# Optimization experiments

Measured on AMD Instinct MI355X. Metric: run time of the kernel, lower is better.

The kernel has to match this reference:

```python
import jax, jax.numpy as jnp
import numpy as np

B, K, V_DIM, EMBED, HID, NTOKEN, MAX_LEN = 128, 36, 2048, 1024, 1024, 10000, 20


def _u(key, shape, scale=0.05):
    return jax.random.uniform(key, shape, jnp.float32, -scale, scale)


def setup_inputs() -> dict:
    key = jax.random.key(0)
    ks = jax.random.split(key, 12)
    d1 = HID + V_DIM + EMBED  # word_rnn input size
    d2 = V_DIM + HID          # language_rnn input size
    return dict(
        v=jax.random.normal(ks[0], (B, K, V_DIM), jnp.float32),
        caption=jax.random.normal(ks[1], (B, MAX_LEN, EMBED), jnp.float32),
        cap_len=jnp.sort(jax.random.randint(ks[2], (B,), 2, MAX_LEN + 1))[::-1].astype(jnp.int32),
        Wih1=_u(ks[3], (3 * HID, d1)), Whh1=_u(ks[4], (3 * HID, HID)),
        bih1=jnp.zeros((3 * HID,), jnp.float32), bhh1=jnp.zeros((3 * HID,), jnp.float32),
        Wih2=_u(ks[5], (3 * HID, d2)), Whh2=_u(ks[6], (3 * HID, HID)),
        bih2=jnp.zeros((3 * HID,), jnp.float32), bhh2=jnp.zeros((3 * HID,), jnp.float32),
        Wv=_u(ks[7], (HID, V_DIM)), bv=jnp.zeros((HID,), jnp.float32),
        Wq=_u(ks[8], (HID, HID)), bq=jnp.zeros((HID,), jnp.float32),
        wa=_u(ks[9], (HID,)), ba=jnp.zeros((), jnp.float32),
        W1=_u(ks[10], (HID, HID)), b1=jnp.zeros((HID,), jnp.float32),
        W2=_u(ks[11], (NTOKEN, HID)), b2=jnp.zeros((NTOKEN,), jnp.float32),
    )


def _gru(x, h, Wih, Whh, bih, bhh):
    # PyTorch GRUCell math, gate order (r, z, n)
    gi = x @ Wih.T + bih
    gh = h @ Whh.T + bhh
    ir, iz, inn = jnp.split(gi, 3, axis=-1)
    hr, hz, hn = jnp.split(gh, 3, axis=-1)
    r = jax.nn.sigmoid(ir + hr)
    z = jax.nn.sigmoid(iz + hz)
    n = jnp.tanh(inn + r * hn)
    return (1.0 - z) * n + z * h


def reference(v, caption, cap_len, Wih1, Whh1, bih1, bhh1, Wih2, Whh2, bih2, bhh2,
              Wv, bv, Wq, bq, wa, ba, W1, b1, W2, b2):
    # sort by caption length, descending (as torch forward does)
    order = jnp.argsort(-cap_len)
    v = v[order]
    caption = caption[order]
    cap_len = cap_len[order]
    v_mean = v.mean(1)                                  # [B, V_DIM]
    vproj = jax.nn.relu(v @ Wv.T + bv)                  # [B, K, HID], hoisted out of time loop

    T = MAX_LEN - 1
    dl = cap_len - 1                                    # decode lengths
    mask = (jnp.arange(T)[:, None] < dl[None, :]).astype(v.dtype)   # [T, B]
    prevs = jnp.swapaxes(caption[:, :T, :], 0, 1)       # [T, B, EMBED]

    def step(carry, xs):
        h1, h2 = carry
        prev, m = xs
        h1n = _gru(jnp.concatenate([h2, v_mean, prev], axis=1), h1, Wih1, Whh1, bih1, bhh1)
        hq = h1n @ W1.T + b1                            # h1_fcnet (dropout = identity in eval)
        # 'base' attention: softmax over objects of w^T(relu(Wv v) * relu(Wq q))
        logits = (vproj * jax.nn.relu(hq @ Wq.T + bq)[:, None, :]) @ wa + ba   # [B, K]
        att = jax.nn.softmax(logits, axis=1)
        att_v = jnp.einsum('bk,bkd->bd', att, v)        # attended image feature
        h2n = _gru(jnp.concatenate([att_v, hq], axis=1), h2, Wih2, Whh2, bih2, bhh2)
        word = h2n @ W2.T + b2                          # [B, NTOKEN]
        return (h1n, h2n), (word * m[:, None], att * m[:, None])

    init = (jnp.zeros((B, HID), v.dtype), jnp.zeros((B, HID), v.dtype))
    _, (words, atts) = jax.lax.scan(step, init, (prevs, mask))
    # pad back to max_len timesteps as the torch output buffer does
    predict = jnp.pad(jnp.swapaxes(words, 0, 1), ((0, 0), (0, 1), (0, 0)))   # [B, MAX_LEN, NTOKEN]
    alphas = jnp.pad(jnp.swapaxes(atts, 0, 1), ((0, 0), (0, 1), (0, 0)))     # [B, MAX_LEN, K]
    return predict, alphas
```

## Files before the change

kernel.cpp:

```cpp
#include <hip/hip_runtime.h>
#include <hip/hip_cooperative_groups.h>

namespace cg = cooperative_groups;

typedef unsigned short u16;
typedef __attribute__((ext_vector_type(8))) short bf16x8;
typedef __attribute__((ext_vector_type(4))) float f32x4;

#define NB 128
#define NOBJ 36
#define VDIM 2048
#define EMB 1024
#define HID 1024
#define NTOK 10000
#define MAXLEN 20
#define T_STEPS 19
#define PRED_STRIDE (MAXLEN * NTOK)
#define ALPHA_OFF ((long)NB * MAXLEN * NTOK)
#define HSZ (NB * HID)

struct Args {
  const float *v, *caption;
  const int *cap_len;
  const float *Wih1, *Whh1, *bih1, *bhh1, *Wih2, *Whh2, *bih2, *bhh2;
  const float *Wv, *bv, *Wq, *bq, *wa, *ba, *W1, *b1, *W2, *b2;
  float *out;
  int *order, *dl;
  u16 *Wih1h, *Whh1h, *Wih2h, *Whh2h, *Wvh, *W2h, *vh, *caph, *capl;
  u16 *Wqh, *Wql, *W1T, *Wih2hql, *Wq1u, *Wih2qu;
  u16 *vproj16;
  float *gv1, *gh2s, *h1f, *h2f, *qf, *gcap, *g1a, *g1c, *g2a, *g2b, *gi2h1;
  float *bq1f, *bf2f;
  u16 *h1hi, *h1lo, *h2hi, *h2lo, *avhi, *avlo, *vmhi, *vmlo;
};

__device__ inline float b2f(u16 h) {
  unsigned u = ((unsigned)h) << 16;
  float f;
  __builtin_memcpy(&f, &u, 4);
  return f;
}
__device__ inline u16 f2b_trunc(float x) {
  unsigned u;
  __builtin_memcpy(&u, &x, 4);
  return (u16)(u >> 16);
}
__device__ inline u16 f2b_rne(float x) {
  unsigned u;
// ... 22 lines not shown
__device__ inline float tanhf_(float x) {
  float e = __expf(-2.f * fabsf(x));
  float t = (1.f - e) / (1.f + e);
  return x >= 0.f ? t : -t;
}
__device__ inline float wred_sum(float x) {
#pragma unroll
  for (int off = 32; off > 0; off >>= 1) x += __shfl_xor(x, off, 64);
  return x;
}
__device__ inline float wred_max(float x) {
#pragma unroll
  for (int off = 32; off > 0; off >>= 1) x = fmaxf(x, __shfl_xor(x, off, 64));
  return x;
}

__device__ inline void cvt_hi(const float *src, u16 *dst, long n, long g0,
                              long gs) {
  for (long i = g0 * 4; i < n; i += gs * 4) {
    float4 f = *(const float4 *)(src + i);
    ushort4 o;
    o.x = f2b_rne(f.x);
    o.y = f2b_rne(f.y);
    o.z = f2b_rne(f.z);
    o.w = f2b_rne(f.w);
    *(ushort4 *)(dst + i) = o;
  }
}
__device__ inline void cvt_split(const float *src, u16 *dhi, u16 *dlo, long n,
                                 long g0, long gs) {
  for (long i = g0 * 4; i < n; i += gs * 4) {
    float4 f = *(const float4 *)(src + i);
    ushort4 h, l;
    split_bf16(f.x, h.x, l.x);
    split_bf16(f.y, h.y, l.y);
    split_bf16(f.z, h.z, l.z);
    split_bf16(f.w, h.w, l.w);
    *(ushort4 *)(dhi + i) = h;
    *(ushort4 *)(dlo + i) = l;
  }
}

#define MMK_BODY                                                               \
  {                                                                            \
    const int ko = ks * 32;                                                    \
    bf16x8 va = ldb8(ah + ko);                                                 \
    bf16x8 vl;                                                                 \
    if constexpr (SPLIT) vl = ldb8(al + ko);                                   \
    _Pragma("unroll") for (int i = 0; i < NT; ++i) {                           \
      bf16x8 vb = ldb8(wr + (long)i * wstride + ko);                           \
      acc[i] = mfma16(va, vb, acc[i]);                                         \
      if constexpr (SPLIT) acc[i] = mfma16(vl, vb, acc[i]);                    \
    }                                                                          \
  }

template <int NT, bool SPLIT>
__device__ inline void mmk(f32x4 *acc, const u16 *ah, const u16 *al,
                           const u16 *wr, long wstride, int ksteps) {
  if constexpr (NT == 1) {
#pragma unroll 4
    for (int ks = 0; ks < ksteps; ++ks) MMK_BODY
  } else {
#pragma unroll 2
    for (int ks = 0; ks < ksteps; ++ks) MMK_BODY
  }
}

template <bool SPLIT>
__device__ inline f32x4 tile16(const u16 *ah, const u16 *al, const u16 *wr,
                               int K) {
  f32x4 acc = {0.f, 0.f, 0.f, 0.f};
  mmk<1, SPLIT>(&acc, ah, al, wr, 0, K >> 5);
  return acc;
}

__global__ void __launch_bounds__(512, 4) butd(Args a) {
  cg::grid_group grid = cg::this_grid();
  const int tid = threadIdx.x;
  const int blk = blockIdx.x;
  const int gx = gridDim.x;
  const int lane = tid & 63;
  const int wv = tid >> 6;
  const int m = lane & 15;
  const int quad = lane >> 4;
  __shared__ float sl[64];

  const long gs = (long)gx * 512;
  const long g0 = (long)blk * 512 + tid;

  cvt_hi(a.Wih1, a.Wih1h, 3072L * 4096, g0, gs);
  cvt_hi(a.Whh1, a.Whh1h, 3072L * 1024, g0, gs);
  cvt_hi(a.Wih2, a.Wih2h, 3072L * 3072, g0, gs);
  cvt_hi(a.Whh2, a.Whh2h, 3072L * 1024, g0, gs);
  cvt_hi(a.Wv, a.Wvh, 1024L * 2048, g0, gs);
  cvt_hi(a.W2, a.W2h, (long)NTOK * 1024, g0, gs);
  cvt_hi(a.v, a.vh, (long)NB * NOBJ * VDIM, g0, gs);
  cvt_split(a.caption, a.caph, a.capl, (long)NB * MAXLEN * EMB, g0, gs);
  cvt_split(a.Wq, a.Wqh, a.Wql, 1024L * 1024, g0, gs);
  for (long i = g0; i < 1024L * 1024; i += gs) {
    const int ii = (int)(i >> 10), mm2 = (int)(i & 1023);
    a.W1T[i] = f2b_rne(a.W1[(long)mm2 * 1024 + ii]);
  }
  for (long i = g0 * 4; i < 3072L * 1024; i += gs * 4) {
    const int row = (int)(i >> 10), c = (int)(i & 1023);
    float4 f = *(const float4 *)(a.Wih2 + (long)row * 3072 + 2048 + c);
    ushort4 l;
    l.x = f2b_trunc(f.x - b2f(f2b_rne(f.x)));
    l.y = f2b_trunc(f.y - b2f(f2b_rne(f.y)));
    l.z = f2b_trunc(f.z - b2f(f2b_rne(f.z)));
    l.w = f2b_trunc(f.w - b2f(f2b_rne(f.w)));
    *(ushort4 *)(a.Wih2hql + i) = l;
  }

  if (blk == 0 && tid < NB) {
    int ki = a.cap_len[tid];
    int rank = 0;
    for (int j = 0; j < NB; ++j) {
      int kj = a.cap_len[j];
      rank += (kj > ki) || (kj == ki && j < tid);
    }
    a.order[rank] = tid;
    a.dl[rank] = ki - 1;
  }
  for (long i = g0; i < (long)NB * NTOK; i += gs) {
    long b = i / NTOK, n = i - b * NTOK;
    a.out[b * PRED_STRIDE + (long)(MAXLEN - 1) * NTOK + n] = 0.f;
  }
  for (long i = g0; i < (long)NB * NOBJ; i += gs) {
    long b = i / NOBJ, n = i - b * NOBJ;
    a.out[ALPHA_OFF + b * (MAXLEN * NOBJ) + (MAXLEN - 1) * NOBJ + n] = 0.f;
  }
  for (long i = g0; i < HSZ; i += gs) {
    a.h1f[i] = 0.f;
    a.h2f[i] = 0.f;
    a.h1hi[i] = 0;
    a.h1lo[i] = 0;
    a.h2hi[i] = 0;
    a.h2lo[i] = 0;
  }
  for (long i = g0; i < 128L * 3072; i += gs) a.g1c[i] = 0.f;
  grid.sync();

  for (int b = blk; b < NB; b += gx) {
    const int ob = a.order[b];
    const float *vb = a.v + (long)ob * NOBJ * VDIM;
    for (int d = tid; d < VDIM; d += 512) {
      float s = 0.f;
      for (int k = 0; k < NOBJ; ++k) s += vb[(long)k * VDIM + d];
      s *= (1.f / 36.f);
      u16 hi, lo;
      split_bf16(s, hi, lo);
      a.vmhi[b * VDIM + d] = hi;
      a.vmlo[b * VDIM + d] = lo;
    }
  }
  for (int tt = blk; tt < 576; tt += gx) {
    const int mg = tt % 36, ngr = tt / 36;
    const int row = mg * 128 + wv * 16 + m;
    const int bb = row / NOBJ, ko = row - bb * NOBJ;
    const u16 *ar = a.vh + ((long)a.order[bb] * NOBJ + ko) * VDIM + quad * 8;
    const int c0 = ngr * 64;
    const u16 *wr = a.Wvh + (long)(c0 + m) * VDIM + quad * 8;
    f32x4 acc[4] = {};
    mmk<4, false>(acc, ar, nullptr, wr, 16L * VDIM, VDIM / 32);
#pragma unroll
    for (int i = 0; i < 4; ++i) {
      const int col = c0 + i * 16 + m;
      const float bvv = a.bv[col];
#pragma unroll
// ... 8 lines not shown
      float s = 0.f;
      for (int c = lane; c < 1024; c += 64) s += a.Wq[(long)o * 1024 + c] * a.b1[c];
      s = wred_sum(s);
      if (lane == 0) a.bq1f[o] = s + a.bq[o];
    } else {
      const int oo = o - 1024;
      float s = 0.f;
      for (int c = lane; c < 1024; c += 64)
        s += a.Wih2[(long)oo * 3072 + 2048 + c] * a.b1[c];
      s = wred_sum(s);
      if (lane == 0) a.bf2f[oo] = s;
    }
  }
  grid.sync();

  {
    const int arow = wv * 16 + m;
    for (int task = blk; task < 5888; task += gx) {
      if (task < 192) {
        const int col = task * 16 + m;
        f32x4 acc = tile16<true>(
            a.vmhi + (long)arow * VDIM + quad * 8,
            a.vmlo + (long)arow * VDIM + quad * 8,
            a.Wih1h + (long)col * 4096 + 1024 + quad * 8, VDIM);
        const float bb = a.bih1[col];
#pragma unroll
        for (int r = 0; r < 4; ++r)
          a.gv1[(long)(wv * 16 + quad * 4 + r) * 3072 + col] = acc[r] + bb;
      } else if (task < 3840) {
        const int tt2 = task - 192;
        const int tdx = tt2 / 192, ct = tt2 % 192;
        const int col = ct * 16 + m;
        const long capoff = ((long)a.order[arow] * MAXLEN + tdx) * EMB;
        f32x4 acc = tile16<true>(
            a.caph + capoff + quad * 8, a.capl + capoff + quad * 8,
            a.Wih1h + (long)col * 4096 + 3072 + quad * 8, EMB);
#pragma unroll
        for (int r = 0; r < 4; ++r)
          a.gcap[((long)tdx * NB + wv * 16 + quad * 4 + r) * 3072 + col] =
              acc[r];
      } else if (task < 4352) {
        const int tt2 = task - 3840;
        const int rg = tt2 >> 6, ct = tt2 & 63;
        const int row = rg * 128 + arow, col = ct * 16 + m;
        f32x4 acc = tile16<true>(a.Wqh + (long)row * HID + quad * 8,
                                 a.Wql + (long)row * HID + quad * 8,
                                 a.W1T + (long)col * HID + quad * 8, HID);
#pragma unroll
        for (int r = 0; r < 4; ++r) {
          const int o = rg * 128 + wv * 16 + quad * 4 + r;
          a.Wq1u[(long)o * HID + col] = f2b_rne(acc[r]);
        }
      } else {
        const int tt2 = task - 4352;
        const int rg = tt2 >> 6, ct = tt2 & 63;
        const int row = rg * 128 + arow, col = ct * 16 + m;
        f32x4 acc = tile16<true>(
            a.Wih2h + (long)row * 3072 + 2048 + quad * 8,
            a.Wih2hql + (long)row * HID + quad * 8,
            a.W1T + (long)col * HID + quad * 8, HID);
#pragma unroll
        for (int r = 0; r < 4; ++r) {
          const int o = rg * 128 + wv * 16 + quad * 4 + r;
          a.Wih2qu[(long)o * HID + col] = f2b_rne(acc[r]);
        }
      }
    }
  }
  grid.sync();

  const int arow = wv * 16 + m;

  auto word_tile = [&](int wt, int tf, int pb) {
    const int col = wt * 16 + m;
    f32x4 acc = tile16<true>(
        a.h2hi + (long)pb * HSZ + (long)arow * HID + quad * 8,
        a.h2lo + (long)pb * HSZ + (long)arow * HID + quad * 8,
        a.W2h + (long)col * HID + quad * 8, HID);
    const float bb = a.b2[col];
#pragma unroll
    for (int r = 0; r < 4; ++r) {
      const int grow = wv * 16 + quad * 4 + r;
      const int msk = tf < a.dl[grow];
      a.out[(long)grow * PRED_STRIDE + (long)tf * NTOK + col] =
          msk ? acc[r] + bb : 0.f;
    }
  };

  auto attention = [&](int t, int b, int half) {
    __syncthreads();
    const int ob = a.order[b];
    const float *qrow = a.qf + (long)b * HID;
    for (int k = wv; k < NOBJ; k += 8) {
      const u16 *vp = a.vproj16 + ((long)b * NOBJ + k) * HID;
      float s = 0.f;
      for (int d = lane; d < HID; d += 64) s += b2f(vp[d]) * qrow[d] * a.wa[d];
      s = wred_sum(s);
      if (lane == 0) sl[k] = s + a.ba[0];
    }
    __syncthreads();
    if (wv == 0) {
      float x = (lane < NOBJ) ? sl[lane] : -3.0e38f;
      float mx = wred_max(x);
      float e = (lane < NOBJ) ? __expf(x - mx) : 0.f;
      float den = wred_sum(e);
      float att = e / den;
      if (lane < NOBJ) {
        sl[lane] = att;
        if (half == 0) {
          const int msk = t < a.dl[b];
          a.out[ALPHA_OFF + (long)b * (MAXLEN * NOBJ) + t * NOBJ + lane] =
              msk ? att : 0.f;
        }
      }
    }
    __syncthreads();
    const u16 *vb = a.vh + (long)ob * NOBJ * VDIM + half * 1024;
    for (int d = tid; d < 1024; d += 512) {
      float s = 0.f;
#pragma unroll
      for (int k = 0; k < NOBJ; ++k) s += sl[k] * b2f(vb[(long)k * VDIM + d]);
      u16 hi, lo;
      split_bf16(s, hi, lo);
      a.avhi[(long)b * VDIM + half * 1024 + d] = hi;
      a.avlo[(long)b * VDIM + half * 1024 + d] = lo;
    }
  };

  auto S1 = [&](int t) {
    const int pr = t & 1;
    const u16 *h2h = a.h2hi + (long)pr * HSZ + (long)arow * HID + quad * 8;
    const u16 *h2l = a.h2lo + (long)pr * HSZ + (long)arow * HID + quad * 8;
    for (int task = blk; task < 512; task += gx) {
      if (task < 192) {
        const int col = task * 16 + m;
        f32x4 acc = tile16<true>(h2h, h2l,
                                 a.Wih1h + (long)col * 4096 + quad * 8, HID);
#pragma unroll
        for (int r = 0; r < 4; ++r)
          a.g1a[(long)(wv * 16 + quad * 4 + r) * 3072 + col] = acc[r];
      } else if (task < 384) {
        const int col = (task - 192) * 16 + m;
        f32x4 acc =
            tile16<true>(h2h, h2l, a.Whh2h + (long)col * HID + quad * 8, HID);
        const float bb = a.bhh2[col];
#pragma unroll
        for (int r = 0; r < 4; ++r)
          a.gh2s[(long)(wv * 16 + quad * 4 + r) * 3072 + col] = acc[r] + bb;
      } else if (t > 0) {
        word_tile(task - 384, t - 1, pr);
      }
    }
  };

  auto S2 = [&](int t) {
    const int pr = t & 1, pw_ = pr ^ 1;
    for (long i = g0; i < (long)HSZ; i += gs) {
      const int row = (int)(i >> 10), col = (int)(i & 1023);
      const long o3 = (long)row * 3072 + col;
      const float *gc = a.gcap + ((long)t * NB + row) * 3072 + col;
      float ir = a.g1a[o3] + gc[0] + a.gv1[o3];
      float iz = a.g1a[o3 + 1024] + gc[1024] + a.gv1[o3 + 1024];
      float in_ = a.g1a[o3 + 2048] + gc[2048] + a.gv1[o3 + 2048];
      float hr = a.g1c[o3] + a.bhh1[col];
      float hz = a.g1c[o3 + 1024] + a.bhh1[HID + col];
      float hn = a.g1c[o3 + 2048] + a.bhh1[2 * HID + col];
      float rr = sigmoidf_(ir + hr);
      float zz = sigmoidf_(iz + hz);
      float nn = tanhf_(in_ + rr * hn);
      const long io = (long)pr * HSZ + i, iw = (long)pw_ * HSZ + i;
      float hnew = (1.f - zz) * nn + zz * a.h1f[io];
      a.h1f[iw] = hnew;
      u16 hi, lo;
      split_bf16(hnew, hi, lo);
      a.h1hi[iw] = hi;
      a.h1lo[iw] = lo;
    }
    if (t > 0)
      for (int task = blk; task < 256; task += gx)
        word_tile(128 + task, t - 1, t & 1);
  };

  auto S3 = [&](int t) {
    const int pw_ = (t & 1) ^ 1;
    const u16 *h1h = a.h1hi + (long)pw_ * HSZ + (long)arow * HID + quad * 8;
    const u16 *h1l = a.h1lo + (long)pw_ * HSZ + (long)arow * HID + quad * 8;
    for (int task = blk; task < 497; task += gx) {
      if (task < 64) {
        const int col = task * 16 + m;
        f32x4 acc =
            tile16<true>(h1h, h1l, a.Wq1u + (long)col * HID + quad * 8, HID);
        const float bb = a.bq1f[col];
#pragma unroll
        for (int r = 0; r < 4; ++r)
          a.qf[(long)(wv * 16 + quad * 4 + r) * HID + col] =
              fmaxf(acc[r] + bb, 0.f);
      } else if (task < 256) {
        const int col = (task - 64) * 16 + m;
        f32x4 acc =
            tile16<true>(h1h, h1l, a.Wih2qu + (long)col * HID + quad * 8, HID);
#pragma unroll
        for (int r = 0; r < 4; ++r)
          a.gi2h1[(long)(wv * 16 + quad * 4 + r) * 3072 + col] = acc[r];
      } else if (t > 0) {
        word_tile(384 + (task - 256), t - 1, t & 1);
      }
    }
  };

  auto S4 = [&](int t) {
    const int pw_ = (t & 1) ^ 1;
    for (int task = blk; task < 448; task += gx) {
      if (task < 256) {
        attention(t, task & 127, task >> 7);
      } else if (t + 1 < T_STEPS) {
        const int col = (task - 256) * 16 + m;
        f32x4 acc = tile16<true>(
            a.h1hi + (long)pw_ * HSZ + (long)arow * HID + quad * 8,
            a.h1lo + (long)pw_ * HSZ + (long)arow * HID + quad * 8,
            a.Whh1h + (long)col * HID + quad * 8, HID);
#pragma unroll
        for (int r = 0; r < 4; ++r)
          a.g1c[(long)(wv * 16 + quad * 4 + r) * 3072 + col] = acc[r];
      }
    }
  };

  auto S5 = [&](int t) {
    (void)t;
    for (int task = blk; task < 384; task += gx) {
      const int kh = task / 192, ct = task % 192;
      const int col = ct * 16 + m;
      f32x4 acc = tile16<true>(
          a.avhi + kh * 1024 + (long)arow * VDIM + quad * 8,
          a.avlo + kh * 1024 + (long)arow * VDIM + quad * 8,
          a.Wih2h + (long)col * 3072 + kh * 1024 + quad * 8, HID);
      float *dst = kh ? a.g2b : a.g2a;
#pragma unroll
      for (int r = 0; r < 4; ++r)
        dst[(long)(wv * 16 + quad * 4 + r) * 3072 + col] = acc[r];
    }
  };

  auto S6 = [&](int t) {
    const int pr = t & 1, pw_ = pr ^ 1;
    for (long i = g0; i < (long)HSZ; i += gs) {
      const int row = (int)(i >> 10), col = (int)(i & 1023);
      const long o3 = (long)row * 3072 + col;
      float ir = a.g2a[o3] + a.g2b[o3] + a.gi2h1[o3] + a.bih2[col] + a.bf2f[col];
      float iz = a.g2a[o3 + 1024] + a.g2b[o3 + 1024] + a.gi2h1[o3 + 1024] +
                 a.bih2[HID + col] + a.bf2f[HID + col];
      float in_ = a.g2a[o3 + 2048] + a.g2b[o3 + 2048] + a.gi2h1[o3 + 2048] +
                  a.bih2[2 * HID + col] + a.bf2f[2 * HID + col];
      float hr = a.gh2s[o3], hz = a.gh2s[o3 + 1024], hn = a.gh2s[o3 + 2048];
      float rr = sigmoidf_(ir + hr);
      float zz = sigmoidf_(iz + hz);
      float nn = tanhf_(in_ + rr * hn);
      const long io = (long)pr * HSZ + i, iw = (long)pw_ * HSZ + i;
      float hnew = (1.f - zz) * nn + zz * a.h2f[io];
      a.h2f[iw] = hnew;
      u16 hi, lo;
      split_bf16(hnew, hi, lo);
      a.h2hi[iw] = hi;
      a.h2lo[iw] = lo;
    }
  };

  for (int t = 0; t < T_STEPS; ++t) {
    S1(t);
    grid.sync();
    S2(t);
    grid.sync();
    S3(t);
    grid.sync();
    S4(t);
    grid.sync();
    S5(t);
    grid.sync();
    S6(t);
// ... 26 lines not shown
  a.W1 = (const float *)d_in[17];
  a.b1 = (const float *)d_in[18];
  a.W2 = (const float *)d_in[19];
  a.b2 = (const float *)d_in[20];
  a.out = (float *)d_out;

  char *w = (char *)d_ws;
  size_t off = 0;
  auto take = [&](size_t bytes) -> void * {
    void *p = w + off;
    off += (bytes + 255) & ~(size_t)255;
    return p;
  };
  a.order = (int *)take(NB * 4);
  a.dl = (int *)take(NB * 4);
  a.Wih1h = (u16 *)take(3072UL * 4096 * 2);
  a.Whh1h = (u16 *)take(3072UL * 1024 * 2);
  a.Wih2h = (u16 *)take(3072UL * 3072 * 2);
  a.Whh2h = (u16 *)take(3072UL * 1024 * 2);
  a.Wvh = (u16 *)take(1024UL * 2048 * 2);
  a.W2h = (u16 *)take((size_t)NTOK * 1024 * 2);
  a.vh = (u16 *)take((size_t)NB * NOBJ * VDIM * 2);
  a.caph = (u16 *)take((size_t)NB * MAXLEN * EMB * 2);
  a.capl = (u16 *)take((size_t)NB * MAXLEN * EMB * 2);
  a.Wqh = (u16 *)take(1024UL * 1024 * 2);
  a.Wql = (u16 *)take(1024UL * 1024 * 2);
  a.W1T = (u16 *)take(1024UL * 1024 * 2);
  a.Wih2hql = (u16 *)take(3072UL * 1024 * 2);
  a.Wq1u = (u16 *)take(1024UL * 1024 * 2);
  a.Wih2qu = (u16 *)take(3072UL * 1024 * 2);
  a.vproj16 = (u16 *)take((size_t)NB * NOBJ * HID * 2);
  a.gv1 = (float *)take((size_t)NB * 3072 * 4);
  a.gh2s = (float *)take((size_t)NB * 3072 * 4);
  a.h1f = (float *)take((size_t)2 * HSZ * 4);
  a.h2f = (float *)take((size_t)2 * HSZ * 4);
  a.qf = (float *)take((size_t)HSZ * 4);
  a.gcap = (float *)take((size_t)T_STEPS * NB * 3072 * 4);
  a.g1a = (float *)take((size_t)NB * 3072 * 4);
  a.g1c = (float *)take((size_t)NB * 3072 * 4);
  a.g2a = (float *)take((size_t)NB * 3072 * 4);
  a.g2b = (float *)take((size_t)NB * 3072 * 4);
  a.gi2h1 = (float *)take((size_t)NB * 3072 * 4);
  a.bq1f = (float *)take(1024UL * 4);
  a.bf2f = (float *)take(3072UL * 4);
  a.h1hi = (u16 *)take((size_t)2 * HSZ * 2);
  a.h1lo = (u16 *)take((size_t)2 * HSZ * 2);
  a.h2hi = (u16 *)take((size_t)2 * HSZ * 2);
  a.h2lo = (u16 *)take((size_t)2 * HSZ * 2);
  a.avhi = (u16 *)take((size_t)NB * VDIM * 2);
  a.avlo = (u16 *)take((size_t)NB * VDIM * 2);
  a.vmhi = (u16 *)take((size_t)NB * VDIM * 2);
  a.vmlo = (u16 *)take((size_t)NB * VDIM * 2);

  static int gridBlocks = 0;
  if (gridBlocks == 0) {
    int occ = 0;
    if (hipOccupancyMaxActiveBlocksPerMultiprocessor(&occ, (const void *)butd,
                                                     512, 0) != hipSuccess ||
        occ < 1)
      occ = 1;
    gridBlocks = (occ >= 2) ? 512 : 256;
  }

  void *kargs[] = {(void *)&a};
  hipLaunchCooperativeKernel((const void *)butd, dim3(gridBlocks), dim3(512),
                             kargs, 0, stream);
}
// ... 1 lines not shown
```

Before: 8.730 ms.

## Pre-pack weights and activations into MFMA fragment layout, add nontemporal IO

Weights (Wih1 slices, Whh1/2, Wih2, W2, fused Wq·W1 products) and per-step activations (h1, h2, attended v, v_mean, captions) are stored in a packed layout matching the 16x16x32 MFMA fragment order. Each lane can then load contiguous 16-byte chunks, which should make loads coalesced and simplify address math in every GEMV tile. The change also adds split hi/lo accumulators, vectorised reductions, nontemporal loads and stores for streaming data, and reassigns word-projection tiles into S5. In exchange it needs more packing work and extra workspace at startup, plus more complex index math that has to stay consistent across all stages.

```diff
diff --git a/kernel.cpp b/kernel.cpp
--- a/kernel.cpp
+++ b/kernel.cpp
@@ -26,12 +26,12 @@
   const float *Wv, *bv, *Wq, *bq, *wa, *ba, *W1, *b1, *W2, *b2;
   float *out;
   int *order, *dl;
-  u16 *Wih1h, *Whh1h, *Wih2h, *Whh2h, *Wvh, *W2h, *vh, *caph, *capl;
-  u16 *Wqh, *Wql, *W1T, *Wih2hql, *Wq1u, *Wih2qu;
-  u16 *vproj16;
-  float *gv1, *gh2s, *h1f, *h2f, *qf, *gcap, *g1a, *g1c, *g2a, *g2b, *gi2h1;
+  u16 *Wvh, *vh, *Wqh, *Wql, *W1T, *Wih2c, *Wih2hql, *vproj16;
+  u16 *W1aP, *W1vP, *W1cP, *Whh1P, *Whh2P, *Wih2aP, *W2P, *Wq1P, *Wih2qP;
+  u16 *capphp, *capplp;
+  u16 *h1hp, *h1lp, *h2hp, *h2lp, *avhp, *avlp, *vmhp, *vmlp;
+  float *gv1, *gh2s, *h1f, *h2f, *gcap, *g1a, *g1c, *g2a, *g2b, *gi2h1, *qf;
   float *bq1f, *bf2f;
-  u16 *h1hi, *h1lo, *h2hi, *h2lo, *avhi, *avlo, *vmhi, *vmlo;
 };
 
 __device__ inline float b2f(u16 h) {
@@ -84,30 +84,63 @@
   for (int off = 32; off > 0; off >>= 1) x = fmaxf(x, __shfl_xor(x, off, 64));
   return x;
 }
+__device__ inline void ntstf(float *p, float v) {
+  __builtin_nontemporal_store(v, p);
+}
+__device__ inline f32x4 ntld4(const float *p) {
+  return __builtin_nontemporal_load((const f32x4 *)p);
+}
 
 __device__ inline void cvt_hi(const float *src, u16 *dst, long n, long g0,
                               long gs) {
   for (long i = g0 * 4; i < n; i += gs * 4) {
-    float4 f = *(const float4 *)(src + i);
+    f32x4 f = ntld4(src + i);
     ushort4 o;
-    o.x = f2b_rne(f.x);
-    o.y = f2b_rne(f.y);
-    o.z = f2b_rne(f.z);
-    o.w = f2b_rne(f.w);
+    o.x = f2b_rne(f[0]);
+    o.y = f2b_rne(f[1]);
+    o.z = f2b_rne(f[2]);
+    o.w = f2b_rne(f[3]);
     *(ushort4 *)(dst + i) = o;
   }
 }
 __device__ inline void cvt_split(const float *src, u16 *dhi, u16 *dlo, long n,
                                  long g0, long gs) {
   for (long i = g0 * 4; i < n; i += gs * 4) {
-    float4 f = *(const float4 *)(src + i);
+    f32x4 f = ntld4(src + i);
     ushort4 h, l;
-    split_bf16(f.x, h.x, l.x);
-    split_bf16(f.y, h.y, l.y);
-    split_bf16(f.z, h.z, l.z);
-    split_bf16(f.w, h.w, l.w);
+    split_bf16(f[0], h.x, l.x);
+    split_bf16(f[1], h.y, l.y);
+    split_bf16(f[2], h.z, l.z);
+    split_bf16(f[3], h.w, l.w);
     *(ushort4 *)(dhi + i) = h;
     *(ushort4 *)(dlo + i) = l;
+  }
+}
+
+__device__ inline void packW(const float *src, u16 *dst, int O, int K, int Ksrc,
+                             int k0, long g0, long gs) {
+  const int kblk = K >> 5;
+  const long nfrag = (long)(O >> 4) * kblk * 64;
+  for (long f = g0; f < nfrag; f += gs) {
+    const int lane_ = (int)(f & 63);
+    const long cgks = f >> 6;
+    const int ks = (int)(cgks % kblk);
+    const int colg = (int)(cgks / kblk);
+    const int col = colg * 16 + (lane_ & 15);
+    const int k = k0 + ks * 32 + (lane_ >> 4) * 8;
+    const float *s = src + (long)col * Ksrc + k;
+    f32x4 f0 = ntld4(s), f1 = ntld4(s + 4);
+    ushort4 o0, o1;
+    o0.x = f2b_rne(f0[0]);
+    o0.y = f2b_rne(f0[1]);
+    o0.z = f2b_rne(f0[2]);
+    o0.w = f2b_rne(f0[3]);
+    o1.x = f2b_rne(f1[0]);
+    o1.y = f2b_rne(f1[1]);
+    o1.z = f2b_rne(f1[2]);
+    o1.w = f2b_rne(f1[3]);
+    *(ushort4 *)(dst + f * 8) = o0;
+    *(ushort4 *)(dst + f * 8 + 4) = o1;
   }
 }
 
@@ -127,21 +160,46 @@
 template <int NT, bool SPLIT>
 __device__ inline void mmk(f32x4 *acc, const u16 *ah, const u16 *al,
                            const u16 *wr, long wstride, int ksteps) {
-  if constexpr (NT == 1) {
-#pragma unroll 4
-    for (int ks = 0; ks < ksteps; ++ks) MMK_BODY
-  } else {
 #pragma unroll 2
-    for (int ks = 0; ks < ksteps; ++ks) MMK_BODY
-  }
+  for (int ks = 0; ks < ksteps; ++ks) MMK_BODY
 }
 
 template <bool SPLIT>
 __device__ inline f32x4 tile16(const u16 *ah, const u16 *al, const u16 *wr,
                                int K) {
-  f32x4 acc = {0.f, 0.f, 0.f, 0.f};
-  mmk<1, SPLIT>(&acc, ah, al, wr, 0, K >> 5);
-  return acc;
+  f32x4 acch = {0.f, 0.f, 0.f, 0.f};
+  f32x4 accl = {0.f, 0.f, 0.f, 0.f};
+  const int ksteps = K >> 5;
+#pragma unroll 4
+  for (int ks = 0; ks < ksteps; ++ks) {
+    const int ko = ks * 32;
+    bf16x8 vb = ldb8(wr + ko);
+    acch = mfma16(ldb8(ah + ko), vb, acch);
+    if constexpr (SPLIT) accl = mfma16(ldb8(al + ko), vb, accl);
+  }
+  if constexpr (SPLIT) {
+#pragma unroll
+    for (int r = 0; r < 4; ++r) acch[r] += accl[r];
+  }
+  return acch;
+}
+
+template <bool SPLIT>
+__device__ inline f32x4 tile16p(const u16 *ah, const u16 *al, const u16 *bp,
+                                int ksteps) {
+  f32x4 acch = {0.f, 0.f, 0.f, 0.f};
+  f32x4 accl = {0.f, 0.f, 0.f, 0.f};
+#pragma unroll 4
+  for (int ks = 0; ks < ksteps; ++ks) {
+    bf16x8 vb = ldb8(bp + ks * 512);
+    acch = mfma16(ldb8(ah + ks * 512), vb, acch);
+    if constexpr (SPLIT) accl = mfma16(ldb8(al + ks * 512), vb, accl);
+  }
+  if constexpr (SPLIT) {
+#pragma unroll
+    for (int r = 0; r < 4; ++r) acch[r] += accl[r];
+  }
+  return acch;
 }
 
 __global__ void __launch_bounds__(512, 4) butd(Args a) {
@@ -158,14 +216,15 @@
   const long gs = (long)gx * 512;
   const long g0 = (long)blk * 512 + tid;
 
-  cvt_hi(a.Wih1, a.Wih1h, 3072L * 4096, g0, gs);
-  cvt_hi(a.Whh1, a.Whh1h, 3072L * 1024, g0, gs);
-  cvt_hi(a.Wih2, a.Wih2h, 3072L * 3072, g0, gs);
-  cvt_hi(a.Whh2, a.Whh2h, 3072L * 1024, g0, gs);
+  packW(a.Wih1, a.W1aP, 3072, 1024, 4096, 0, g0, gs);
+  packW(a.Wih1, a.W1vP, 3072, 2048, 4096, 1024, g0, gs);
+  packW(a.Wih1, a.W1cP, 3072, 1024, 4096, 3072, g0, gs);
+  packW(a.Whh1, a.Whh1P, 3072, 1024, 1024, 0, g0, gs);
+  packW(a.Whh2, a.Whh2P, 3072, 1024, 1024, 0, g0, gs);
+  packW(a.Wih2, a.Wih2aP, 3072, 2048, 3072, 0, g0, gs);
+  packW(a.W2, a.W2P, NTOK, 1024, 1024, 0, g0, gs);
   cvt_hi(a.Wv, a.Wvh, 1024L * 2048, g0, gs);
-  cvt_hi(a.W2, a.W2h, (long)NTOK * 1024, g0, gs);
   cvt_hi(a.v, a.vh, (long)NB * NOBJ * VDIM, g0, gs);
-  cvt_split(a.caption, a.caph, a.capl, (long)NB * MAXLEN * EMB, g0, gs);
   cvt_split(a.Wq, a.Wqh, a.Wql, 1024L * 1024, g0, gs);
   for (long i = g0; i < 1024L * 1024; i += gs) {
     const int ii = (int)(i >> 10), mm2 = (int)(i & 1023);
@@ -173,12 +232,17 @@
   }
   for (long i = g0 * 4; i < 3072L * 1024; i += gs * 4) {
     const int row = (int)(i >> 10), c = (int)(i & 1023);
-    float4 f = *(const float4 *)(a.Wih2 + (long)row * 3072 + 2048 + c);
-    ushort4 l;
-    l.x = f2b_trunc(f.x - b2f(f2b_rne(f.x)));
-    l.y = f2b_trunc(f.y - b2f(f2b_rne(f.y)));
-    l.z = f2b_trunc(f.z - b2f(f2b_rne(f.z)));
-    l.w = f2b_trunc(f.w - b2f(f2b_rne(f.w)));
+    f32x4 f = ntld4(a.Wih2 + (long)row * 3072 + 2048 + c);
+    ushort4 h, l;
+    h.x = f2b_rne(f[0]);
+    h.y = f2b_rne(f[1]);
+    h.z = f2b_rne(f[2]);
+    h.w = f2b_rne(f[3]);
+    l.x = f2b_trunc(f[0] - b2f(h.x));
+    l.y = f2b_trunc(f[1] - b2f(h.y));
+    l.z = f2b_trunc(f[2] - b2f(h.z));
+    l.w = f2b_trunc(f[3] - b2f(h.w));
+    *(ushort4 *)(a.Wih2c + i) = h;
     *(ushort4 *)(a.Wih2hql + i) = l;
   }
 
@@ -194,35 +258,83 @@
   }
   for (long i = g0; i < (long)NB * NTOK; i += gs) {
     long b = i / NTOK, n = i - b * NTOK;
-    a.out[b * PRED_STRIDE + (long)(MAXLEN - 1) * NTOK + n] = 0.f;
+    ntstf(&a.out[b * PRED_STRIDE + (long)(MAXLEN - 1) * NTOK + n], 0.f);
   }
   for (long i = g0; i < (long)NB * NOBJ; i += gs) {
     long b = i / NOBJ, n = i - b * NOBJ;
-    a.out[ALPHA_OFF + b * (MAXLEN * NOBJ) + (MAXLEN - 1) * NOBJ + n] = 0.f;
+    ntstf(&a.out[ALPHA_OFF + b * (MAXLEN * NOBJ) + (MAXLEN - 1) * NOBJ + n],
+          0.f);
   }
   for (long i = g0; i < HSZ; i += gs) {
     a.h1f[i] = 0.f;
     a.h2f[i] = 0.f;
-    a.h1hi[i] = 0;
-    a.h1lo[i] = 0;
-    a.h2hi[i] = 0;
-    a.h2lo[i] = 0;
+    a.h1hp[i] = 0;
+    a.h1lp[i] = 0;
+    a.h2hp[i] = 0;
+    a.h2lp[i] = 0;
   }
   for (long i = g0; i < 128L * 3072; i += gs) a.g1c[i] = 0.f;
   grid.sync();
 
   for (int b = blk; b < NB; b += gx) {
     const int ob = a.order[b];
-    const float *vb = a.v + (long)ob * NOBJ * VDIM;
-    for (int d = tid; d < VDIM; d += 512) {
-      float s = 0.f;
-      for (int k = 0; k < NOBJ; ++k) s += vb[(long)k * VDIM + d];
-      s *= (1.f / 36.f);
-      u16 hi, lo;
-      split_bf16(s, hi, lo);
-      a.vmhi[b * VDIM + d] = hi;
-      a.vmlo[b * VDIM + d] = lo;
-    }
+    if (tid < 256) {
+      const int d0 = tid * 8;
+      const float *vb = a.v + (long)ob * NOBJ * VDIM + d0;
+      float s[8] = {};
+      for (int k = 0; k < NOBJ; ++k) {
+        f32x4 x0 = *(const f32x4 *)(vb + (long)k * VDIM);
+        f32x4 x1 = *(const f32x4 *)(vb + (long)k * VDIM + 4);
+#pragma unroll
+        for (int j = 0; j < 4; ++j) {
+          s[j] += x0[j];
+          s[4 + j] += x1[j];
+        }
+      }
+      ushort4 H0, H1, L0, L1;
+#pragma unroll
+      for (int j = 0; j < 8; ++j) s[j] *= (1.f / 36.f);
+      split_bf16(s[0], H0.x, L0.x);
+      split_bf16(s[1], H0.y, L0.y);
+      split_bf16(s[2], H0.z, L0.z);
+      split_bf16(s[3], H0.w, L0.w);
+      split_bf16(s[4], H1.x, L1.x);
+      split_bf16(s[5], H1.y, L1.y);
+      split_bf16(s[6], H1.z, L1.z);
+      split_bf16(s[7], H1.w, L1.w);
+      const long po = (((long)(b >> 4) * 64 + (d0 >> 5)) * 64 +
+                       ((d0 >> 3) & 3) * 16 + (b & 15)) *
+                      8;
+      *(ushort4 *)(a.vmhp + po) = H0;
+      *(ushort4 *)(a.vmhp + po + 4) = H1;
+      *(ushort4 *)(a.vmlp + po) = L0;
+      *(ushort4 *)(a.vmlp + po + 4) = L1;
+    }
+  }
+  for (long f = g0; f < 19L * 8 * 32 * 64; f += gs) {
+    const int lane_ = (int)(f & 63);
+    long rest = f >> 6;
+    const int ks = (int)(rest & 31);
+    rest >>= 5;
+    const int tile = (int)(rest & 7);
+    const int t = (int)(rest >> 3);
+    const int b = a.order[tile * 16 + (lane_ & 15)];
+    const int k = ks * 32 + (lane_ >> 4) * 8;
+    const float *s = a.caption + ((long)b * MAXLEN + t) * EMB + k;
+    f32x4 f0 = ntld4(s), f1 = ntld4(s + 4);
+    ushort4 H0, H1, L0, L1;
+    split_bf16(f0[0], H0.x, L0.x);
+    split_bf16(f0[1], H0.y, L0.y);
+    split_bf16(f0[2], H0.z, L0.z);
+    split_bf16(f0[3], H0.w, L0.w);
+    split_bf16(f1[0], H1.x, L1.x);
+    split_bf16(f1[1], H1.y, L1.y);
+    split_bf16(f1[2], H1.z, L1.z);
+    split_bf16(f1[3], H1.w, L1.w);
+    *(ushort4 *)(a.capphp + f * 8) = H0;
+    *(ushort4 *)(a.capphp + f * 8 + 4) = H1;
+    *(ushort4 *)(a.capplp + f * 8) = L0;
+    *(ushort4 *)(a.capplp + f * 8 + 4) = L1;
   }
   for (int tt = blk; tt < 576; tt += gx) {
     const int mg = tt % 36, ngr = tt / 36;
@@ -261,76 +373,72 @@
   }
   grid.sync();
 
-  {
-    const int arow = wv * 16 + m;
-    for (int task = blk; task < 5888; task += gx) {
-      if (task < 192) {
-        const int col = task * 16 + m;
-        f32x4 acc = tile16<true>(
-            a.vmhi + (long)arow * VDIM + quad * 8,
-            a.vmlo + (long)arow * VDIM + quad * 8,
-            a.Wih1h + (long)col * 4096 + 1024 + quad * 8, VDIM);
-        const float bb = a.bih1[col];
-#pragma unroll
-        for (int r = 0; r < 4; ++r)
-          a.gv1[(long)(wv * 16 + quad * 4 + r) * 3072 + col] = acc[r] + bb;
-      } else if (task < 3840) {
-        const int tt2 = task - 192;
-        const int tdx = tt2 / 192, ct = tt2 % 192;
-        const int col = ct * 16 + m;
-        const long capoff = ((long)a.order[arow] * MAXLEN + tdx) * EMB;
-        f32x4 acc = tile16<true>(
-            a.caph + capoff + quad * 8, a.capl + capoff + quad * 8,
-            a.Wih1h + (long)col * 4096 + 3072 + quad * 8, EMB);
-#pragma unroll
-        for (int r = 0; r < 4; ++r)
-          a.gcap[((long)tdx * NB + wv * 16 + quad * 4 + r) * 3072 + col] =
-              acc[r];
-      } else if (task < 4352) {
-        const int tt2 = task - 3840;
-        const int rg = tt2 >> 6, ct = tt2 & 63;
-        const int row = rg * 128 + arow, col = ct * 16 + m;
-        f32x4 acc = tile16<true>(a.Wqh + (long)row * HID + quad * 8,
-                                 a.Wql + (long)row * HID + quad * 8,
-                                 a.W1T + (long)col * HID + quad * 8, HID);
-#pragma unroll
-        for (int r = 0; r < 4; ++r) {
-          const int o = rg * 128 + wv * 16 + quad * 4 + r;
-          a.Wq1u[(long)o * HID + col] = f2b_rne(acc[r]);
-        }
-      } else {
-        const int tt2 = task - 4352;
-        const int rg = tt2 >> 6, ct = tt2 & 63;
-        const int row = rg * 128 + arow, col = ct * 16 + m;
-        f32x4 acc = tile16<true>(
-            a.Wih2h + (long)row * 3072 + 2048 + quad * 8,
-            a.Wih2hql + (long)row * HID + quad * 8,
-            a.W1T + (long)col * HID + quad * 8, HID);
-#pragma unroll
-        for (int r = 0; r < 4; ++r) {
-          const int o = rg * 128 + wv * 16 + quad * 4 + r;
-          a.Wih2qu[(long)o * HID + col] = f2b_rne(acc[r]);
-        }
+  for (int task = blk; task < 5888; task += gx) {
+    if (task < 192) {
+      const u16 *ah = a.vmhp + (long)wv * 64 * 512 + lane * 8;
+      const u16 *al = a.vmlp + (long)wv * 64 * 512 + lane * 8;
+      f32x4 acc = tile16p<true>(ah, al,
+                                a.W1vP + (long)task * 64 * 512 + lane * 8, 64);
+      const int col = task * 16 + m;
+      const float bb = a.bih1[col];
+#pragma unroll
+      for (int r = 0; r < 4; ++r)
+        a.gv1[(long)(wv * 16 + quad * 4 + r) * 3072 + col] = acc[r] + bb;
+    } else if (task < 3840) {
+      const int tt2 = task - 192;
+      const int tdx = tt2 / 192, ct = tt2 % 192;
+      const u16 *ah = a.capphp + ((long)(tdx * 8 + wv) * 32) * 512 + lane * 8;
+      const u16 *al = a.capplp + ((long)(tdx * 8 + wv) * 32) * 512 + lane * 8;
+      f32x4 acc =
+          tile16p<true>(ah, al, a.W1cP + (long)ct * 32 * 512 + lane * 8, 32);
+      const int col = ct * 16 + m;
+#pragma unroll
+      for (int r = 0; r < 4; ++r)
+        a.gcap[((long)tdx * NB + wv * 16 + quad * 4 + r) * 3072 + col] = acc[r];
+    } else if (task < 4352) {
+      const int tt2 = task - 3840;
+      const int rg = tt2 >> 6, ct = tt2 & 63;
+      const int row = rg * 128 + wv * 16 + m, col = ct * 16 + m;
+      f32x4 acc = tile16<true>(a.Wqh + (long)row * HID + quad * 8,
+                               a.Wql + (long)row * HID + quad * 8,
+                               a.W1T + (long)col * HID + quad * 8, HID);
+#pragma unroll
+      for (int r = 0; r < 4; ++r) {
+        const int n = rg * 128 + wv * 16 + quad * 4 + r;
+        a.Wq1P[((long)(n >> 4) * 32 + (col >> 5)) * 512 +
+               (((col >> 3) & 3) * 16 + (n & 15)) * 8 + (col & 7)] =
+            f2b_rne(acc[r]);
+      }
+    } else {
+      const int tt2 = task - 4352;
+      const int rg = tt2 >> 6, ct = tt2 & 63;
+      const int row = rg * 128 + wv * 16 + m, col = ct * 16 + m;
+      f32x4 acc = tile16<true>(a.Wih2c + (long)row * 1024 + quad * 8,
+                               a.Wih2hql + (long)row * 1024 + quad * 8,
+                               a.W1T + (long)col * HID + quad * 8, HID);
+#pragma unroll
+      for (int r = 0; r < 4; ++r) {
+        const int n = rg * 128 + wv * 16 + quad * 4 + r;
+        a.Wih2qP[((long)(n >> 4) * 32 + (col >> 5)) * 512 +
+                 (((col >> 3) & 3) * 16 + (n & 15)) * 8 + (col & 7)] =
+            f2b_rne(acc[r]);
       }
     }
   }
   grid.sync();
 
-  const int arow = wv * 16 + m;
-
   auto word_tile = [&](int wt, int tf, int pb) {
+    const long ab = ((long)(pb * 8 + wv) * 32) * 512 + lane * 8;
+    f32x4 acc = tile16p<true>(a.h2hp + ab, a.h2lp + ab,
+                              a.W2P + (long)wt * 32 * 512 + lane * 8, 32);
     const int col = wt * 16 + m;
-    f32x4 acc = tile16<true>(
-        a.h2hi + (long)pb * HSZ + (long)arow * HID + quad * 8,
-        a.h2lo + (long)pb * HSZ + (long)arow * HID + quad * 8,
-        a.W2h + (long)col * HID + quad * 8, HID);
     const float bb = a.b2[col];
 #pragma unroll
     for (int r = 0; r < 4; ++r) {
       const int grow = wv * 16 + quad * 4 + r;
       const int msk = tf < a.dl[grow];
-      a.out[(long)grow * PRED_STRIDE + (long)tf * NTOK + col] =
-          msk ? acc[r] + bb : 0.f;
+      ntstf(&a.out[(long)grow * PRED_STRIDE + (long)tf * NTOK + col],
+            msk ? acc[r] + bb : 0.f);
     }
   };
 
@@ -356,40 +464,59 @@
         sl[lane] = att;
         if (half == 0) {
           const int msk = t < a.dl[b];
-          a.out[ALPHA_OFF + (long)b * (MAXLEN * NOBJ) + t * NOBJ + lane] =
-              msk ? att : 0.f;
+          ntstf(&a.out[ALPHA_OFF + (long)b * (MAXLEN * NOBJ) + t * NOBJ + lane],
+                msk ? att : 0.f);
         }
       }
     }
     __syncthreads();
-    const u16 *vb = a.vh + (long)ob * NOBJ * VDIM + half * 1024;
-    for (int d = tid; d < 1024; d += 512) {
-      float s = 0.f;
-#pragma unroll
-      for (int k = 0; k < NOBJ; ++k) s += sl[k] * b2f(vb[(long)k * VDIM + d]);
-      u16 hi, lo;
-      split_bf16(s, hi, lo);
-      a.avhi[(long)b * VDIM + half * 1024 + d] = hi;
-      a.avlo[(long)b * VDIM + half * 1024 + d] = lo;
+    if (tid < 128) {
+      const int d0 = half * 1024 + tid * 8;
+      const u16 *vb = a.vh + (long)ob * NOBJ * VDIM + d0;
+      float s[8] = {};
+      for (int k = 0; k < NOBJ; ++k) {
+        bf16x8 vv = ldb8(vb + (long)k * VDIM);
+        const float w = sl[k];
+#pragma unroll
+        for (int j = 0; j < 8; ++j) s[j] += w * b2f((u16)vv[j]);
+      }
+      ushort4 H0, H1, L0, L1;
+      split_bf16(s[0], H0.x, L0.x);
+      split_bf16(s[1], H0.y, L0.y);
+      split_bf16(s[2], H0.z, L0.z);
+      split_bf16(s[3], H0.w, L0.w);
+      split_bf16(s[4], H1.x, L1.x);
+      split_bf16(s[5], H1.y, L1.y);
+      split_bf16(s[6], H1.z, L1.z);
+      split_bf16(s[7], H1.w, L1.w);
+      const long po = (((long)(b >> 4) * 64 + (d0 >> 5)) * 64 +
+                       ((d0 >> 3) & 3) * 16 + (b & 15)) *
+                      8;
+      *(ushort4 *)(a.avhp + po) = H0;
+      *(ushort4 *)(a.avhp + po + 4) = H1;
+      *(ushort4 *)(a.avlp + po) = L0;
+      *(ushort4 *)(a.avlp + po + 4) = L1;
     }
   };
 
   auto S1 = [&](int t) {
     const int pr = t & 1;
-    const u16 *h2h = a.h2hi + (long)pr * HSZ + (long)arow * HID + quad * 8;
-    const u16 *h2l = a.h2lo + (long)pr * HSZ + (long)arow * HID + quad * 8;
+    const long ab = ((long)(pr * 8 + wv) * 32) * 512 + lane * 8;
+    const u16 *h2h = a.h2hp + ab;
+    const u16 *h2l = a.h2lp + ab;
     for (int task = blk; task < 512; task += gx) {
       if (task < 192) {
+        f32x4 acc = tile16p<true>(
+            h2h, h2l, a.W1aP + (long)task * 32 * 512 + lane * 8, 32);
         const int col = task * 16 + m;
-        f32x4 acc = tile16<true>(h2h, h2l,
-                                 a.Wih1h + (long)col * 4096 + quad * 8, HID);
 #pragma unroll
         for (int r = 0; r < 4; ++r)
           a.g1a[(long)(wv * 16 + quad * 4 + r) * 3072 + col] = acc[r];
       } else if (task < 384) {
-        const int col = (task - 192) * 16 + m;
-        f32x4 acc =
-            tile16<true>(h2h, h2l, a.Whh2h + (long)col * HID + quad * 8, HID);
+        const int ct = task - 192;
+        f32x4 acc = tile16p<true>(
+            h2h, h2l, a.Whh2P + (long)ct * 32 * 512 + lane * 8, 32);
+        const int col = ct * 16 + m;
         const float bb = a.bhh2[col];
 #pragma unroll
         for (int r = 0; r < 4; ++r)
@@ -402,55 +529,77 @@
 
   auto S2 = [&](int t) {
     const int pr = t & 1, pw_ = pr ^ 1;
-    for (long i = g0; i < (long)HSZ; i += gs) {
-      const int row = (int)(i >> 10), col = (int)(i & 1023);
-      const long o3 = (long)row * 3072 + col;
-      const float *gc = a.gcap + ((long)t * NB + row) * 3072 + col;
-      float ir = a.g1a[o3] + gc[0] + a.gv1[o3];
-      float iz = a.g1a[o3 + 1024] + gc[1024] + a.gv1[o3 + 1024];
-      float in_ = a.g1a[o3 + 2048] + gc[2048] + a.gv1[o3 + 2048];
-      float hr = a.g1c[o3] + a.bhh1[col];
-      float hz = a.g1c[o3 + 1024] + a.bhh1[HID + col];
-      float hn = a.g1c[o3 + 2048] + a.bhh1[2 * HID + col];
-      float rr = sigmoidf_(ir + hr);
-      float zz = sigmoidf_(iz + hz);
-      float nn = tanhf_(in_ + rr * hn);
-      const long io = (long)pr * HSZ + i, iw = (long)pw_ * HSZ + i;
-      float hnew = (1.f - zz) * nn + zz * a.h1f[io];
-      a.h1f[iw] = hnew;
-      u16 hi, lo;
-      split_bf16(hnew, hi, lo);
-      a.h1hi[iw] = hi;
-      a.h1lo[iw] = lo;
+    const int bi = gx - 1 - blk;
+    if (bi < 32) {
+      const int chunk = bi * 512 + tid;
+      const int row = chunk >> 7, k0 = (chunk & 127) * 8;
+      const long o3 = (long)row * 3072 + k0;
+      const float *gc = a.gcap + ((long)t * NB + row) * 3072 + k0;
+      const long io = (long)pr * HSZ + (long)row * HID + k0;
+      const long iw = (long)pw_ * HSZ + (long)row * HID + k0;
+      float hn8[8];
+#pragma unroll
+      for (int j = 0; j < 8; ++j) {
+        const int col = k0 + j;
+        float ir = a.g1a[o3 + j] + gc[j] + a.gv1[o3 + j];
+        float iz = a.g1a[o3 + 1024 + j] + gc[1024 + j] + a.gv1[o3 + 1024 + j];
+        float in_ = a.g1a[o3 + 2048 + j] + gc[2048 + j] + a.gv1[o3 + 2048 + j];
+        float hr = a.g1c[o3 + j] + a.bhh1[col];
+        float hz = a.g1c[o3 + 1024 + j] + a.bhh1[HID + col];
+        float hn = a.g1c[o3 + 2048 + j] + a.bhh1[2 * HID + col];
+        float rr = sigmoidf_(ir + hr);
+        float zz = sigmoidf_(iz + hz);
+        float nn = tanhf_(in_ + rr * hn);
+        hn8[j] = (1.f - zz) * nn + zz * a.h1f[io + j];
+        a.h1f[iw + j] = hn8[j];
+      }
+      ushort4 H0, H1, L0, L1;
+      split_bf16(hn8[0], H0.x, L0.x);
+      split_bf16(hn8[1], H0.y, L0.y);
+      split_bf16(hn8[2], H0.z, L0.z);
+      split_bf16(hn8[3], H0.w, L0.w);
+      split_bf16(hn8[4], H1.x, L1.x);
+      split_bf16(hn8[5], H1.y, L1.y);
+      split_bf16(hn8[6], H1.z, L1.z);
+      split_bf16(hn8[7], H1.w, L1.w);
+      const long po = (((long)(pw_ * 8 + (row >> 4)) * 32 + (k0 >> 5)) * 64 +
+                       ((k0 >> 3) & 3) * 16 + (row & 15)) *
+                      8;
+      *(ushort4 *)(a.h1hp + po) = H0;
+      *(ushort4 *)(a.h1hp + po + 4) = H1;
+      *(ushort4 *)(a.h1lp + po) = L0;
+      *(ushort4 *)(a.h1lp + po + 4) = L1;
     }
     if (t > 0)
-      for (int task = blk; task < 256; task += gx)
-        word_tile(128 + task, t - 1, t & 1);
+      for (int task = blk; task < 320; task += gx)
+        word_tile(128 + task, t - 1, pr);
   };
 
   auto S3 = [&](int t) {
     const int pw_ = (t & 1) ^ 1;
-    const u16 *h1h = a.h1hi + (long)pw_ * HSZ + (long)arow * HID + quad * 8;
-    const u16 *h1l = a.h1lo + (long)pw_ * HSZ + (long)arow * HID + quad * 8;
-    for (int task = blk; task < 497; task += gx) {
+    const long ab = ((long)(pw_ * 8 + wv) * 32) * 512 + lane * 8;
+    const u16 *h1h = a.h1hp + ab;
+    const u16 *h1l = a.h1lp + ab;
+    for (int task = blk; task < 381; task += gx) {
       if (task < 64) {
+        f32x4 acc = tile16p<true>(
+            h1h, h1l, a.Wq1P + (long)task * 32 * 512 + lane * 8, 32);
         const int col = task * 16 + m;
-        f32x4 acc =
-            tile16<true>(h1h, h1l, a.Wq1u + (long)col * HID + quad * 8, HID);
         const float bb = a.bq1f[col];
 #pragma unroll
         for (int r = 0; r < 4; ++r)
           a.qf[(long)(wv * 16 + quad * 4 + r) * HID + col] =
               fmaxf(acc[r] + bb, 0.f);
       } else if (task < 256) {
-        const int col = (task - 64) * 16 + m;
-        f32x4 acc =
-            tile16<true>(h1h, h1l, a.Wih2qu + (long)col * HID + quad * 8, HID);
+        const int ct = task - 64;
+        f32x4 acc = tile16p<true>(
+            h1h, h1l, a.Wih2qP + (long)ct * 32 * 512 + lane * 8, 32);
+        const int col = ct * 16 + m;
 #pragma unroll
         for (int r = 0; r < 4; ++r)
           a.gi2h1[(long)(wv * 16 + quad * 4 + r) * 3072 + col] = acc[r];
       } else if (t > 0) {
-        word_tile(384 + (task - 256), t - 1, t & 1);
+        word_tile(448 + (task - 256), t - 1, t & 1);
       }
     }
   };
@@ -461,11 +610,11 @@
       if (task < 256) {
         attention(t, task & 127, task >> 7);
       } else if (t + 1 < T_STEPS) {
-        const int col = (task - 256) * 16 + m;
-        f32x4 acc = tile16<true>(
-            a.h1hi + (long)pw_ * HSZ + (long)arow * HID + quad * 8,
-            a.h1lo + (long)pw_ * HSZ + (long)arow * HID + quad * 8,
-            a.Whh1h + (long)col * HID + quad * 8, HID);
+        const int ct = task - 256;
+        const long ab = ((long)(pw_ * 8 + wv) * 32) * 512 + lane * 8;
+        f32x4 acc = tile16p<true>(a.h1hp + ab, a.h1lp + ab,
+                                  a.Whh1P + (long)ct * 32 * 512 + lane * 8, 32);
+        const int col = ct * 16 + m;
 #pragma unroll
         for (int r = 0; r < 4; ++r)
           a.g1c[(long)(wv * 16 + quad * 4 + r) * 3072 + col] = acc[r];
@@ -474,42 +623,69 @@
   };
 
   auto S5 = [&](int t) {
-    (void)t;
-    for (int task = blk; task < 384; task += gx) {
-      const int kh = task / 192, ct = task % 192;
-      const int col = ct * 16 + m;
-      f32x4 acc = tile16<true>(
-          a.avhi + kh * 1024 + (long)arow * VDIM + quad * 8,
-          a.avlo + kh * 1024 + (long)arow * VDIM + quad * 8,
-          a.Wih2h + (long)col * 3072 + kh * 1024 + quad * 8, HID);
-      float *dst = kh ? a.g2b : a.g2a;
-#pragma unroll
-      for (int r = 0; r < 4; ++r)
-        dst[(long)(wv * 16 + quad * 4 + r) * 3072 + col] = acc[r];
+    for (int task = blk; task < 436; task += gx) {
+      if (task < 384) {
+        const int kh = task / 192, ct = task % 192;
+        const long aoff = ((long)wv * 64 + kh * 32) * 512 + lane * 8;
+        f32x4 acc = tile16p<true>(
+            a.avhp + aoff, a.avlp + aoff,
+            a.Wih2aP + ((long)ct * 64 + kh * 32) * 512 + lane * 8, 32);
+        float *dst = kh ? a.g2b : a.g2a;
+        const int col = ct * 16 + m;
+#pragma unroll
+        for (int r = 0; r < 4; ++r)
+          dst[(long)(wv * 16 + quad * 4 + r) * 3072 + col] = acc[r];
+      } else if (t > 0) {
+        word_tile(573 + (task - 384), t - 1, t & 1);
+      }
     }
   };
 
   auto S6 = [&](int t) {
     const int pr = t & 1, pw_ = pr ^ 1;
-    for (long i = g0; i < (long)HSZ; i += gs) {
-      const int row = (int)(i >> 10), col = (int)(i & 1023);
-      const long o3 = (long)row * 3072 + col;
-      float ir = a.g2a[o3] + a.g2b[o3] + a.gi2h1[o3] + a.bih2[col] + a.bf2f[col];
-      float iz = a.g2a[o3 + 1024] + a.g2b[o3 + 1024] + a.gi2h1[o3 + 1024] +
-                 a.bih2[HID + col] + a.bf2f[HID + col];
-      float in_ = a.g2a[o3 + 2048] + a.g2b[o3 + 2048] + a.gi2h1[o3 + 2048] +
-                  a.bih2[2 * HID + col] + a.bf2f[2 * HID + col];
-      float hr = a.gh2s[o3], hz = a.gh2s[o3 + 1024], hn = a.gh2s[o3 + 2048];
-      float rr = sigmoidf_(ir + hr);
-      float zz = sigmoidf_(iz + hz);
-      float nn = tanhf_(in_ + rr * hn);
-      const long io = (long)pr * HSZ + i, iw = (long)pw_ * HSZ + i;
-      float hnew = (1.f - zz) * nn + zz * a.h2f[io];
-      a.h2f[iw] = hnew;
-      u16 hi, lo;
-      split_bf16(hnew, hi, lo);
-      a.h2hi[iw] = hi;
-      a.h2lo[iw] = lo;
+    const int bi = gx - 1 - blk;
+    if (bi < 32) {
+      const int chunk = bi * 512 + tid;
+      const int row = chunk >> 7, k0 = (chunk & 127) * 8;
+      const long o3 = (long)row * 3072 + k0;
+      const long io = (long)pr * HSZ + (long)row * HID + k0;
+      const long iw = (long)pw_ * HSZ + (long)row * HID + k0;
+      float hn8[8];
+#pragma unroll
+      for (int j = 0; j < 8; ++j) {
+        const int col = k0 + j;
+        float ir = a.g2a[o3 + j] + a.g2b[o3 + j] + a.gi2h1[o3 + j] +
+                   a.bih2[col] + a.bf2f[col];
+        float iz = a.g2a[o3 + 1024 + j] + a.g2b[o3 + 1024 + j] +
+                   a.gi2h1[o3 + 1024 + j] + a.bih2[HID + col] +
+                   a.bf2f[HID + col];
+        float in_ = a.g2a[o3 + 2048 + j] + a.g2b[o3 + 2048 + j] +
+                    a.gi2h1[o3 + 2048 + j] + a.bih2[2 * HID + col] +
+                    a.bf2f[2 * HID + col];
+        float hr = a.gh2s[o3 + j], hz = a.gh2s[o3 + 1024 + j],
+              hn = a.gh2s[o3 + 2048 + j];
+        float rr = sigmoidf_(ir + hr);
+        float zz = sigmoidf_(iz + hz);
+        float nn = tanhf_(in_ + rr * hn);
+        hn8[j] = (1.f - zz) * nn + zz * a.h2f[io + j];
+        a.h2f[iw + j] = hn8[j];
+      }
+      ushort4 H0, H1, L0, L1;
+      split_bf16(hn8[0], H0.x, L0.x);
+      split_bf16(hn8[1], H0.y, L0.y);
+      split_bf16(hn8[2], H0.z, L0.z);
+      split_bf16(hn8[3], H0.w, L0.w);
+      split_bf16(hn8[4], H1.x, L1.x);
+      split_bf16(hn8[5], H1.y, L1.y);
+      split_bf16(hn8[6], H1.z, L1.z);
+      split_bf16(hn8[7], H1.w, L1.w);
+      const long po = (((long)(pw_ * 8 + (row >> 4)) * 32 + (k0 >> 5)) * 64 +
+                       ((k0 >> 3) & 3) * 16 + (row & 15)) *
+                      8;
+      *(ushort4 *)(a.h2hp + po) = H0;
+      *(ushort4 *)(a.h2hp + po + 4) = H1;
+      *(ushort4 *)(a.h2lp + po) = L0;
+      *(ushort4 *)(a.h2lp + po + 4) = L1;
     }
   };
 
@@ -566,22 +742,33 @@
   };
   a.order = (int *)take(NB * 4);
   a.dl = (int *)take(NB * 4);
-  a.Wih1h = (u16 *)take(3072UL * 4096 * 2);
-  a.Whh1h = (u16 *)take(3072UL * 1024 * 2);
-  a.Wih2h = (u16 *)take(3072UL * 3072 * 2);
-  a.Whh2h = (u16 *)take(3072UL * 1024 * 2);
+  a.W1aP = (u16 *)take(3072UL * 1024 * 2);
+  a.W1vP = (u16 *)take(3072UL * 2048 * 2);
+  a.W1cP = (u16 *)take(3072UL * 1024 * 2);
+  a.Whh1P = (u16 *)take(3072UL * 1024 * 2);
+  a.Whh2P = (u16 *)take(3072UL * 1024 * 2);
+  a.Wih2aP = (u16 *)take(3072UL * 2048 * 2);
+  a.W2P = (u16 *)take((size_t)NTOK * 1024 * 2);
+  a.Wq1P = (u16 *)take(1024UL * 1024 * 2);
+  a.Wih2qP = (u16 *)take(3072UL * 1024 * 2);
+  a.capphp = (u16 *)take(19UL * 8 * 32 * 512 * 2);
+  a.capplp = (u16 *)take(19UL * 8 * 32 * 512 * 2);
   a.Wvh = (u16 *)take(1024UL * 2048 * 2);
-  a.W2h = (u16 *)take((size_t)NTOK * 1024 * 2);
   a.vh = (u16 *)take((size_t)NB * NOBJ * VDIM * 2);
-  a.caph = (u16 *)take((size_t)NB * MAXLEN * EMB * 2);
-  a.capl = (u16 *)take((size_t)NB * MAXLEN * EMB * 2);
   a.Wqh = (u16 *)take(1024UL * 1024 * 2);
   a.Wql = (u16 *)take(1024UL * 1024 * 2);
   a.W1T = (u16 *)take(1024UL * 1024 * 2);
+  a.Wih2c = (u16 *)take(3072UL * 1024 * 2);
   a.Wih2hql = (u16 *)take(3072UL * 1024 * 2);
-  a.Wq1u = (u16 *)take(1024UL * 1024 * 2);
-  a.Wih2qu = (u16 *)take(3072UL * 1024 * 2);
   a.vproj16 = (u16 *)take((size_t)NB * NOBJ * HID * 2);
+  a.h1hp = (u16 *)take(2UL * 8 * 32 * 512 * 2);
+  a.h1lp = (u16 *)take(2UL * 8 * 32 * 512 * 2);
+  a.h2hp = (u16 *)take(2UL * 8 * 32 * 512 * 2);
+  a.h2lp = (u16 *)take(2UL * 8 * 32 * 512 * 2);
+  a.avhp = (u16 *)take(8UL * 64 * 512 * 2);
+  a.avlp = (u16 *)take(8UL * 64 * 512 * 2);
+  a.vmhp = (u16 *)take(8UL * 64 * 512 * 2);
+  a.vmlp = (u16 *)take(8UL * 64 * 512 * 2);
   a.gv1 = (float *)take((size_t)NB * 3072 * 4);
   a.gh2s = (float *)take((size_t)NB * 3072 * 4);
   a.h1f = (float *)take((size_t)2 * HSZ * 4);
@@ -595,14 +782,6 @@
   a.gi2h1 = (float *)take((size_t)NB * 3072 * 4);
   a.bq1f = (float *)take(1024UL * 4);
   a.bf2f = (float *)take(3072UL * 4);
-  a.h1hi = (u16 *)take((size_t)2 * HSZ * 2);
-  a.h1lo = (u16 *)take((size_t)2 * HSZ * 2);
-  a.h2hi = (u16 *)take((size_t)2 * HSZ * 2);
-  a.h2lo = (u16 *)take((size_t)2 * HSZ * 2);
-  a.avhi = (u16 *)take((size_t)NB * VDIM * 2);
-  a.avlo = (u16 *)take((size_t)NB * VDIM * 2);
-  a.vmhi = (u16 *)take((size_t)NB * VDIM * 2);
-  a.vmlo = (u16 *)take((size_t)NB * VDIM * 2);
 
   static int gridBlocks = 0;
   if (gridBlocks == 0) {
```

New measurement: 9.022 ms. 3.3% more time.
